# Performance work log

Measured on AMD Instinct MI355X. Metric: run time of the kernel, lower is better.

## Reference

```python
import jax, jax.numpy as jnp
import numpy as np

SCALE = 1.0  # noise std used in the Gaussian log-pdf
HIGH = jax.lax.Precision.HIGHEST


def setup_inputs() -> dict:
    key = jax.random.key(0)
    k1, k2, k3 = jax.random.split(key, 3)
    B, N, D, T = 64, 256, 64, 4096
    data = jax.random.normal(k1, (B, N, D), dtype=jnp.float32)
    targets = jax.random.normal(k2, (B, N), dtype=jnp.float32)
    task_pool = jax.random.normal(k3, (T, D, 1), dtype=jnp.float32)
    return {"data": data, "targets": targets, "task_pool": task_pool}


def reference(data, targets, task_pool):
    # data: [B, N, D], targets: [B, N], task_pool: [T, D, 1]
    W = jnp.squeeze(task_pool).T  # [D, T]
    # Per-point, per-task Gaussian log-likelihood of targets under each task weight.
    Z = jnp.einsum('bnd,dt->bnt', data, W, precision=HIGH)  # [B, N, T]
    resid = targets[:, :, None] - Z
    logp = jax.scipy.stats.norm.logpdf(resid, loc=0.0, scale=SCALE)  # [B, N, T]
    # alpha for step i (i >= 1) is the cumulative log-lik over points 0..i-1.
    cum = jnp.cumsum(logp, axis=1)          # [B, N, T]
    alphas = cum[:, :-1]                    # [B, N-1, T], alphas[:, i-1] = alpha at step i
    post = jax.nn.softmax(alphas, axis=-1)  # posterior over tasks per step
    # MMSE weight per step: posterior-weighted average of task weights.
    w_mmse = jnp.einsum('bit,dt->bid', post, W, precision=HIGH)  # [B, N-1, D]
    preds_rest = jnp.einsum('bid,bid->bi', data[:, 1:], w_mmse)  # [B, N-1]
    # Step 0: prior mean weight (uniform average over task pool).
    pred0 = data[:, 0] @ W.mean(axis=1)  # [B]
    return jnp.concatenate([pred0[:, None], preds_rest], axis=1)  # [B, N]
```

## Files before the change

### kernel.cpp

```cpp
#include <hip/hip_runtime.h>
#include <math.h>

#define BB 64
#define NN 256
#define DD 64
#define TT 4096

#define NCH 16
#define CT (TT/NCH)
#define THREADS 512
#define WAVES 8
#define NB 16
#define NGRP (NN/NB)
#define BN (BB*NN)

typedef __bf16 bf16x8 __attribute__((ext_vector_type(8)));
typedef float  f32x4  __attribute__((ext_vector_type(4)));

#define SHR1 0x111
#define SHR2 0x112
#define SHR4 0x114
#define SHR8 0x118
#define ROR1 0x121
#define ROR2 0x122
#define ROR4 0x124
#define ROR8 0x128

template<int C>
__device__ __forceinline__ float dppf(float x) {
  return __int_as_float(__builtin_amdgcn_update_dpp(
      0, __float_as_int(x), C, 0xf, 0xf, true));
}

__device__ __forceinline__ unsigned short f2bf(float f) {
  unsigned int u = __float_as_uint(f);
  unsigned int r = u + 0x7FFFu + ((u >> 16) & 1u);
  return (unsigned short)(r >> 16);
}
__device__ __forceinline__ float bf2f(unsigned short h) {
  return __uint_as_float(((unsigned int)h) << 16);
}

union FragU { unsigned int u[4]; bf16x8 v; };

__device__ __forceinline__ void merge8(const float4 (*sb)[16], int lane,
                                       float* __restrict__ part, size_t obase) {
  const int col = lane & 15;
  float4 p0 = sb[0][col];
  float M = p0.x, S = p0.y, V = p0.z;
  #pragma unroll
  for (int w = 1; w < WAVES; ++w) {
    float4 pw = sb[w][col];
    float mn = fmaxf(M, pw.x);
    float ea = __expf(M - mn), eb = __expf(pw.x - mn);
    S = fmaf(S, ea, pw.y * eb);
    V = fmaf(V, ea, pw.z * eb);
    M = mn;
  }
  if (lane < 16) {
    const size_t o = (obase + col) * 3;
    part[o] = M; part[o + 1] = S; part[o + 2] = V;
  }
}

__global__ __launch_bounds__(THREADS, 4)
void mmse_phase1(const float* __restrict__ data,
                 const float* __restrict__ targets,
                 const float* __restrict__ Wp,
                 float* __restrict__ part)
{
  const int bx   = blockIdx.x;
  const int b    = bx >> 4;
  const int ch   = bx & 15;
  const int tid  = threadIdx.x;
  const int lane = tid & 63;
  const int wave = tid >> 6;

  __shared__ unsigned int sDH[2][2][64][4];
  __shared__ unsigned int sDL[2][2][64][4];
  __shared__ float4 sbuf[2][WAVES][16];

  bf16x8 aH[2][2], aL[2][2];
  {
    const int tb = ch * CT + wave * 32;
    #pragma unroll
    for (int tile = 0; tile < 2; ++tile) {
      #pragma unroll
      for (int s = 0; s < 2; ++s) {
        const int row = tb + tile * 16 + (lane & 15);
        const int kb  = s * 32 + (lane >> 4) * 8;
        const float* wp = Wp + (size_t)row * DD + kb;
        FragU hu, lu;
        #pragma unroll
        for (int jj = 0; jj < 4; ++jj) {
          const float f0 = wp[2 * jj], f1 = wp[2 * jj + 1];
          const unsigned short h0 = f2bf(f0), h1 = f2bf(f1);
          const unsigned short g0 = f2bf(f0 - bf2f(h0)), g1 = f2bf(f1 - bf2f(h1));
          hu.u[jj] = (unsigned int)h0 | ((unsigned int)h1 << 16);
          lu.u[jj] = (unsigned int)g0 | ((unsigned int)g1 << 16);
        }
        aH[tile][s] = hu.v; aL[tile][s] = lu.v;
      }
    }
  }

  const float* __restrict__ dbase = data + (size_t)b * NN * DD;
  const int sn = tid >> 5, sk2 = tid & 31;
  const int ss = sk2 >> 4, sjp = sk2 & 3;
  const int sl = ((sk2 >> 2) & 3) * 16 + sn;

  {
    const float2 q0 = *(const float2*)(dbase + (size_t)sn * DD + sk2 * 2);
    const unsigned short h0 = f2bf(q0.x), h1 = f2bf(q0.y);
    const unsigned short g0 = f2bf(q0.x - bf2f(h0)), g1 = f2bf(q0.y - bf2f(h1));
    sDH[0][ss][sl][sjp] = (unsigned int)h0 | ((unsigned int)h1 << 16);
    sDL[0][ss][sl][sjp] = (unsigned int)g0 | ((unsigned int)g1 << 16);
  }
  __syncthreads();

  float c8[2][4];
  #pragma unroll
  for (int t8 = 0; t8 < 8; ++t8) c8[t8 >> 2][t8 & 3] = 0.f;

  const size_t obase0 = (size_t)ch * BN + (size_t)b * NN;

  #pragma unroll 1
  for (int g = 0; g < NGRP; ++g) {
    const int buf = g & 1;
    bf16x8 bh0 = *(const bf16x8*)&sDH[buf][0][lane][0];
    bf16x8 bh1 = *(const bf16x8*)&sDH[buf][1][lane][0];
    bf16x8 bl0 = *(const bf16x8*)&sDL[buf][0][lane][0];
    bf16x8 bl1 = *(const bf16x8*)&sDL[buf][1][lane][0];

    float2 q;
    if (g + 1 < NGRP)
      q = *(const float2*)(dbase + (size_t)((g + 1) * NB + sn) * DD + sk2 * 2);

    if (g > 0 && wave == ((g - 1) & 7))
      merge8(sbuf[(g - 1) & 1], lane, part, obase0 + (size_t)(g - 1) * NB);

    f32x4 zz[2];
    zz[0] = (f32x4)(0.f); zz[1] = (f32x4)(0.f);
    zz[0] = __builtin_amdgcn_mfma_f32_16x16x32_bf16(aH[0][0], bh0, zz[0], 0, 0, 0);
    zz[0] = __builtin_amdgcn_mfma_f32_16x16x32_bf16(aH[0][0], bl0, zz[0], 0, 0, 0);
    zz[0] = __builtin_amdgcn_mfma_f32_16x16x32_bf16(aL[0][0], bh0, zz[0], 0, 0, 0);
    zz[0] = __builtin_amdgcn_mfma_f32_16x16x32_bf16(aH[0][1], bh1, zz[0], 0, 0, 0);
    zz[0] = __builtin_amdgcn_mfma_f32_16x16x32_bf16(aH[0][1], bl1, zz[0], 0, 0, 0);
    zz[0] = __builtin_amdgcn_mfma_f32_16x16x32_bf16(aL[0][1], bh1, zz[0], 0, 0, 0);
    zz[1] = __builtin_amdgcn_mfma_f32_16x16x32_bf16(aH[1][0], bh0, zz[1], 0, 0, 0);
    zz[1] = __builtin_amdgcn_mfma_f32_16x16x32_bf16(aH[1][0], bl0, zz[1], 0, 0, 0);
    zz[1] = __builtin_amdgcn_mfma_f32_16x16x32_bf16(aL[1][0], bh0, zz[1], 0, 0, 0);
    zz[1] = __builtin_amdgcn_mfma_f32_16x16x32_bf16(aH[1][1], bh1, zz[1], 0, 0, 0);
    zz[1] = __builtin_amdgcn_mfma_f32_16x16x32_bf16(aH[1][1], bl1, zz[1], 0, 0, 0);
    zz[1] = __builtin_amdgcn_mfma_f32_16x16x32_bf16(aL[1][1], bh1, zz[1], 0, 0, 0);

    const float tg = targets[(size_t)b * NN + g * NB + (lane & 15)];
    float alpha[8];
    float mloc = -3.4e38f;
    #pragma unroll
    for (int t8 = 0; t8 < 8; ++t8) {
      const int tile = t8 >> 2, r = t8 & 3;
      const float z = zz[tile][r];
      const float resid = tg - z;
      const float lp = resid * (resid * -0.5f);
      float x = dppf<SHR1>(lp);
      x += dppf<SHR1>(x);
      x += dppf<SHR2>(x);
      x += dppf<SHR4>(x);
      x += dppf<SHR8>(x);
      float tot = lp;
      tot += dppf<ROR1>(tot);
      tot += dppf<ROR2>(tot);
      tot += dppf<ROR4>(tot);
      tot += dppf<ROR8>(tot);
      const float a_ = c8[tile][r] + x;
      alpha[t8] = a_;
      c8[tile][r] += tot;
      mloc = fmaxf(mloc, a_);
    }
    float m = fmaxf(mloc, __shfl_xor(mloc, 16));
    m = fmaxf(m, __shfl_xor(m, 32));
    float sv = 0.f, vv = 0.f;
    #pragma unroll
    for (int t8 = 0; t8 < 8; ++t8) {
      const float p = __expf(alpha[t8] - m);
      sv += p;
      vv = fmaf(p, zz[t8 >> 2][t8 & 3], vv);
    }
    sv += __shfl_xor(sv, 16); sv += __shfl_xor(sv, 32);
    vv += __shfl_xor(vv, 16); vv += __shfl_xor(vv, 32);
    if (lane < 16) sbuf[buf][wave][lane] = make_float4(m, sv, vv, 0.f);

    if (g + 1 < NGRP) {
      const unsigned short h0 = f2bf(q.x), h1 = f2bf(q.y);
      const unsigned short g0 = f2bf(q.x - bf2f(h0)), g1 = f2bf(q.y - bf2f(h1));
      sDH[buf ^ 1][ss][sl][sjp] = (unsigned int)h0 | ((unsigned int)h1 << 16);
      sDL[buf ^ 1][ss][sl][sjp] = (unsigned int)g0 | ((unsigned int)g1 << 16);
    }
    __syncthreads();
  }

  if (wave == ((NGRP - 1) & 7))
    merge8(sbuf[(NGRP - 1) & 1], lane, part, obase0 + (size_t)(NGRP - 1) * NB);
}

__global__ __launch_bounds__(256)
void mmse_phase2(const float* __restrict__ part, float* __restrict__ out)
{
  const int idx = blockIdx.x * 256 + threadIdx.x;
  float M = -3.4e38f, S = 0.f, V = 0.f;
  #pragma unroll
  for (int ch = 0; ch < NCH; ++ch) {
    const size_t o = ((size_t)ch * BN + idx) * 3;
    const float m2 = part[o], s2 = part[o + 1], v2 = part[o + 2];
    const float mn = fmaxf(M, m2);
    const float ea = __expf(M - mn), eb = __expf(m2 - mn);
    S = fmaf(S, ea, s2 * eb);
    V = fmaf(V, ea, v2 * eb);
    M = mn;
  }
  out[idx] = V / S;
}

extern "C" void kernel_launch(void* const* d_in, const int* in_sizes, int n_in,
                              void* d_out, int out_size, void* d_ws, size_t ws_size,
                              hipStream_t stream)
{
  const float* data      = (const float*)d_in[0];
  const float* targets   = (const float*)d_in[1];
  const float* task_pool = (const float*)d_in[2];
  float* out  = (float*)d_out;
  float* part = (float*)d_ws;

  hipLaunchKernelGGL(mmse_phase1, dim3(BB * NCH), dim3(THREADS), 0, stream,
                     data, targets, task_pool, part);
  hipLaunchKernelGGL(mmse_phase2, dim3(BN / 256), dim3(256), 0, stream,
                     part, out);
}
```

Measured before the change: 130.4 us.

## Pre-split data into swizzled bf16 tiles and stream them with global_load_lds

Adds a pre-pass kernel that converts data once into hi/lo bf16 tiles with an XOR-swizzled layout. Previously each of the 16 task-chunk blocks redid this conversion per batch. The main kernel now copies those tiles straight into LDS with async global_load_lds double-buffering, and stages targets in LDS. It also works in base-2 exponent space, gets the inclusive/total scans from one DPP scan plus a swizzle broadcast, and stores normalized (logsum, mean) pairs in a channel-contiguous layout so phase2 can read them coalesced with two threads per output. The cost is an extra launch plus an extra 2 MB tile write and read through workspace.

```diff
diff --git a/kernel.cpp b/kernel.cpp
--- a/kernel.cpp
+++ b/kernel.cpp
@@ -14,6 +14,11 @@
 #define NGRP (NN/NB)
 #define BN (BB*NN)
 
+#define TILE_BYTES 4096
+#define TILES_BYTES ((size_t)BB*NGRP*TILE_BYTES)
+
+#define NHL2E (-0.72134752044448170368f)
+
 typedef __bf16 bf16x8 __attribute__((ext_vector_type(8)));
 typedef float  f32x4  __attribute__((ext_vector_type(4)));
 
@@ -21,10 +26,6 @@
 #define SHR2 0x112
 #define SHR4 0x114
 #define SHR8 0x118
-#define ROR1 0x121
-#define ROR2 0x122
-#define ROR4 0x124
-#define ROR8 0x128
 
 template<int C>
 __device__ __forceinline__ float dppf(float x) {
@@ -32,6 +33,10 @@
       0, __float_as_int(x), C, 0xf, 0xf, true));
 }
 
+__device__ __forceinline__ float bcast15(float x) {
+  return __int_as_float(__builtin_amdgcn_ds_swizzle(__float_as_int(x), 0x1F0));
+}
+
 __device__ __forceinline__ unsigned short f2bf(float f) {
   unsigned int u = __float_as_uint(f);
   unsigned int r = u + 0x7FFFu + ((u >> 16) & 1u);
@@ -41,30 +46,54 @@
   return __uint_as_float(((unsigned int)h) << 16);
 }
 
+#define GLOAD_LDS16(gp, lp_) \
+  __builtin_amdgcn_global_load_lds((const __attribute__((address_space(1))) void*)(gp), \
+                                   (__attribute__((address_space(3))) void*)(lp_), 16, 0, 0)
+
 union FragU { unsigned int u[4]; bf16x8 v; };
 
-__device__ __forceinline__ void merge8(const float4 (*sb)[16], int lane,
+__global__ __launch_bounds__(256)
+void mmse_phase0(const float* __restrict__ data, unsigned char* __restrict__ tiles)
+{
+  const int e  = blockIdx.x * 256 + threadIdx.x;
+  const int k2 = e & 31;
+  const int n  = (e >> 5) & 255;
+  const int b  = e >> 13;
+  const float2 q = ((const float2*)data)[e];
+  const unsigned short h0 = f2bf(q.x), h1 = f2bf(q.y);
+  const unsigned short g0 = f2bf(q.x - bf2f(h0)), g1 = f2bf(q.y - bf2f(h1));
+  const int nr = n & 15;
+  const int logical = nr * 128 + k2 * 4;
+  const int phys = logical ^ ((nr & 7) << 4);
+  unsigned char* tp = tiles + (size_t)(b * NGRP + (n >> 4)) * TILE_BYTES;
+  *(unsigned int*)(tp + phys)        = (unsigned int)h0 | ((unsigned int)h1 << 16);
+  *(unsigned int*)(tp + 2048 + phys) = (unsigned int)g0 | ((unsigned int)g1 << 16);
+}
+
+__device__ __forceinline__ void merge8(const float2 (*sb)[16], int lane,
                                        float* __restrict__ part, size_t obase) {
   const int col = lane & 15;
-  float4 p0 = sb[0][col];
-  float M = p0.x, S = p0.y, V = p0.z;
+  float2 p0 = sb[0][col];
+  float M = p0.x, S = 1.f, V = p0.y;
   #pragma unroll
   for (int w = 1; w < WAVES; ++w) {
-    float4 pw = sb[w][col];
+    float2 pw = sb[w][col];
     float mn = fmaxf(M, pw.x);
-    float ea = __expf(M - mn), eb = __expf(pw.x - mn);
-    S = fmaf(S, ea, pw.y * eb);
-    V = fmaf(V, ea, pw.z * eb);
+    float ea = __builtin_amdgcn_exp2f(M - mn);
+    float eb = __builtin_amdgcn_exp2f(pw.x - mn);
+    S = S * ea + eb;
+    V = fmaf(V, ea, pw.y * eb);
     M = mn;
   }
   if (lane < 16) {
-    const size_t o = (obase + col) * 3;
-    part[o] = M; part[o + 1] = S; part[o + 2] = V;
+    const size_t o = (obase + (size_t)col * NCH) * 2;
+    part[o]     = M + __log2f(S);
+    part[o + 1] = V / S;
   }
 }
 
 __global__ __launch_bounds__(THREADS, 4)
-void mmse_phase1(const float* __restrict__ data,
+void mmse_phase1(const unsigned char* __restrict__ tiles,
                  const float* __restrict__ targets,
                  const float* __restrict__ Wp,
                  float* __restrict__ part)
@@ -76,9 +105,11 @@
   const int lane = tid & 63;
   const int wave = tid >> 6;
 
-  __shared__ unsigned int sDH[2][2][64][4];
-  __shared__ unsigned int sDL[2][2][64][4];
-  __shared__ float4 sbuf[2][WAVES][16];
+  __shared__ uint4  dbufq[2][256];
+  __shared__ float  tgl[NN];
+  __shared__ float2 sbuf[2][WAVES][16];
+
+  unsigned char* dbufc = (unsigned char*)dbufq;
 
   bf16x8 aH[2][2], aL[2][2];
   {
@@ -104,40 +135,35 @@
     }
   }
 
-  const float* __restrict__ dbase = data + (size_t)b * NN * DD;
-  const int sn = tid >> 5, sk2 = tid & 31;
-  const int ss = sk2 >> 4, sjp = sk2 & 3;
-  const int sl = ((sk2 >> 2) & 3) * 16 + sn;
-
-  {
-    const float2 q0 = *(const float2*)(dbase + (size_t)sn * DD + sk2 * 2);
-    const unsigned short h0 = f2bf(q0.x), h1 = f2bf(q0.y);
-    const unsigned short g0 = f2bf(q0.x - bf2f(h0)), g1 = f2bf(q0.y - bf2f(h1));
-    sDH[0][ss][sl][sjp] = (unsigned int)h0 | ((unsigned int)h1 << 16);
-    sDL[0][ss][sl][sjp] = (unsigned int)g0 | ((unsigned int)g1 << 16);
-  }
+  if (wave == 0)
+    GLOAD_LDS16(targets + (size_t)b * NN + lane * 4, tgl);
+  if (wave < 4)
+    GLOAD_LDS16(tiles + (size_t)(b * NGRP) * TILE_BYTES + wave * 1024 + lane * 16,
+                dbufc + wave * 1024);
   __syncthreads();
 
-  float c8[2][4];
+  float c8[8];
   #pragma unroll
-  for (int t8 = 0; t8 < 8; ++t8) c8[t8 >> 2][t8 & 3] = 0.f;
-
-  const size_t obase0 = (size_t)ch * BN + (size_t)b * NN;
+  for (int i = 0; i < 8; ++i) c8[i] = 0.f;
+
+  const size_t obase0 = (size_t)(b * NN) * NCH + ch;
 
   #pragma unroll 1
   for (int g = 0; g < NGRP; ++g) {
     const int buf = g & 1;
-    bf16x8 bh0 = *(const bf16x8*)&sDH[buf][0][lane][0];
-    bf16x8 bh1 = *(const bf16x8*)&sDH[buf][1][lane][0];
-    bf16x8 bl0 = *(const bf16x8*)&sDL[buf][0][lane][0];
-    bf16x8 bl1 = *(const bf16x8*)&sDL[buf][1][lane][0];
-
-    float2 q;
-    if (g + 1 < NGRP)
-      q = *(const float2*)(dbase + (size_t)((g + 1) * NB + sn) * DD + sk2 * 2);
+    const unsigned char* bp = dbufc + buf * 4096;
+    const int ra = ((lane & 15) * 128 + (lane >> 4) * 16) ^ ((lane & 7) << 4);
+    bf16x8 bh0 = *(const bf16x8*)(bp + ra);
+    bf16x8 bh1 = *(const bf16x8*)(bp + (ra ^ 64));
+    bf16x8 bl0 = *(const bf16x8*)(bp + 2048 + ra);
+    bf16x8 bl1 = *(const bf16x8*)(bp + 2048 + (ra ^ 64));
+
+    if (g + 1 < NGRP && wave < 4)
+      GLOAD_LDS16(tiles + (size_t)(b * NGRP + g + 1) * TILE_BYTES + wave * 1024 + lane * 16,
+                  dbufc + (buf ^ 1) * 4096 + wave * 1024);
 
     if (g > 0 && wave == ((g - 1) & 7))
-      merge8(sbuf[(g - 1) & 1], lane, part, obase0 + (size_t)(g - 1) * NB);
+      merge8(sbuf[(g - 1) & 1], lane, part, obase0 + (size_t)((g - 1) * NB) * NCH);
 
     f32x4 zz[2];
     zz[0] = (f32x4)(0.f); zz[1] = (f32x4)(0.f);
@@ -154,72 +180,83 @@
     zz[1] = __builtin_amdgcn_mfma_f32_16x16x32_bf16(aH[1][1], bl1, zz[1], 0, 0, 0);
     zz[1] = __builtin_amdgcn_mfma_f32_16x16x32_bf16(aL[1][1], bh1, zz[1], 0, 0, 0);
 
-    const float tg = targets[(size_t)b * NN + g * NB + (lane & 15)];
+    const float tgf = tgl[g * 16 + (lane & 15)];
+
     float alpha[8];
     float mloc = -3.4e38f;
     #pragma unroll
-    for (int t8 = 0; t8 < 8; ++t8) {
-      const int tile = t8 >> 2, r = t8 & 3;
-      const float z = zz[tile][r];
-      const float resid = tg - z;
-      const float lp = resid * (resid * -0.5f);
-      float x = dppf<SHR1>(lp);
-      x += dppf<SHR1>(x);
-      x += dppf<SHR2>(x);
-      x += dppf<SHR4>(x);
-      x += dppf<SHR8>(x);
-      float tot = lp;
-      tot += dppf<ROR1>(tot);
-      tot += dppf<ROR2>(tot);
-      tot += dppf<ROR4>(tot);
-      tot += dppf<ROR8>(tot);
-      const float a_ = c8[tile][r] + x;
-      alpha[t8] = a_;
-      c8[tile][r] += tot;
-      mloc = fmaxf(mloc, a_);
+    for (int tile = 0; tile < 2; ++tile) {
+      #pragma unroll
+      for (int r = 0; r < 4; ++r) {
+        const int t8 = tile * 4 + r;
+        const float z  = zz[tile][r];
+        const float rr = tgf - z;
+        const float lp = rr * rr * NHL2E;
+        float x = lp;
+        x += dppf<SHR1>(x);
+        x += dppf<SHR2>(x);
+        x += dppf<SHR4>(x);
+        x += dppf<SHR8>(x);
+        const float tot = bcast15(x);
+        const float a_ = c8[t8] + (x - lp);
+        alpha[t8] = a_;
+        c8[t8] += tot;
+        mloc = fmaxf(mloc, a_);
+      }
     }
     float m = fmaxf(mloc, __shfl_xor(mloc, 16));
     m = fmaxf(m, __shfl_xor(m, 32));
     float sv = 0.f, vv = 0.f;
     #pragma unroll
-    for (int t8 = 0; t8 < 8; ++t8) {
-      const float p = __expf(alpha[t8] - m);
-      sv += p;
-      vv = fmaf(p, zz[t8 >> 2][t8 & 3], vv);
+    for (int tile = 0; tile < 2; ++tile) {
+      #pragma unroll
+      for (int r = 0; r < 4; ++r) {
+        const float p = __builtin_amdgcn_exp2f(alpha[tile * 4 + r] - m);
+        sv += p;
+        vv = fmaf(p, zz[tile][r], vv);
+      }
     }
     sv += __shfl_xor(sv, 16); sv += __shfl_xor(sv, 32);
     vv += __shfl_xor(vv, 16); vv += __shfl_xor(vv, 32);
-    if (lane < 16) sbuf[buf][wave][lane] = make_float4(m, sv, vv, 0.f);
-
-    if (g + 1 < NGRP) {
-      const unsigned short h0 = f2bf(q.x), h1 = f2bf(q.y);
-      const unsigned short g0 = f2bf(q.x - bf2f(h0)), g1 = f2bf(q.y - bf2f(h1));
-      sDH[buf ^ 1][ss][sl][sjp] = (unsigned int)h0 | ((unsigned int)h1 << 16);
-      sDL[buf ^ 1][ss][sl][sjp] = (unsigned int)g0 | ((unsigned int)g1 << 16);
-    }
+    if (lane < 16) {
+      float2 lr;
+      lr.x = m + __log2f(sv);
+      lr.y = vv / sv;
+      sbuf[buf][wave][lane] = lr;
+    }
+
     __syncthreads();
   }
 
   if (wave == ((NGRP - 1) & 7))
-    merge8(sbuf[(NGRP - 1) & 1], lane, part, obase0 + (size_t)(NGRP - 1) * NB);
+    merge8(sbuf[(NGRP - 1) & 1], lane, part, obase0 + (size_t)((NGRP - 1) * NB) * NCH);
 }
 
 __global__ __launch_bounds__(256)
 void mmse_phase2(const float* __restrict__ part, float* __restrict__ out)
 {
-  const int idx = blockIdx.x * 256 + threadIdx.x;
+  const int gid  = blockIdx.x * 256 + threadIdx.x;
+  const int idx  = gid >> 1;
+  const int half = gid & 1;
+  const float2* __restrict__ p = (const float2*)part + (size_t)idx * NCH + half * 8;
   float M = -3.4e38f, S = 0.f, V = 0.f;
   #pragma unroll
-  for (int ch = 0; ch < NCH; ++ch) {
-    const size_t o = ((size_t)ch * BN + idx) * 3;
-    const float m2 = part[o], s2 = part[o + 1], v2 = part[o + 2];
-    const float mn = fmaxf(M, m2);
-    const float ea = __expf(M - mn), eb = __expf(m2 - mn);
-    S = fmaf(S, ea, s2 * eb);
-    V = fmaf(V, ea, v2 * eb);
+  for (int c = 0; c < 8; ++c) {
+    const float2 q = p[c];
+    const float mn = fmaxf(M, q.x);
+    const float ea = __builtin_amdgcn_exp2f(M - mn);
+    const float eb = __builtin_amdgcn_exp2f(q.x - mn);
+    S = fmaf(S, ea, eb);
+    V = fmaf(V, ea, q.y * eb);
     M = mn;
   }
-  out[idx] = V / S;
+  const float m2 = __shfl_xor(M, 1), s2 = __shfl_xor(S, 1), v2 = __shfl_xor(V, 1);
+  const float mn = fmaxf(M, m2);
+  const float ea = __builtin_amdgcn_exp2f(M - mn);
+  const float eb = __builtin_amdgcn_exp2f(m2 - mn);
+  S = fmaf(S, ea, s2 * eb);
+  V = fmaf(V, ea, v2 * eb);
+  if (half == 0) out[idx] = V / S;
 }
 
 extern "C" void kernel_launch(void* const* d_in, const int* in_sizes, int n_in,
@@ -229,11 +266,15 @@
   const float* data      = (const float*)d_in[0];
   const float* targets   = (const float*)d_in[1];
   const float* task_pool = (const float*)d_in[2];
-  float* out  = (float*)d_out;
-  float* part = (float*)d_ws;
-
+  float* out = (float*)d_out;
+
+  unsigned char* tiles = (unsigned char*)d_ws;
+  float* part = (float*)((unsigned char*)d_ws + TILES_BYTES);
+
+  hipLaunchKernelGGL(mmse_phase0, dim3(BB * NN * DD / 2 / 256), dim3(256), 0, stream,
+                     data, tiles);
   hipLaunchKernelGGL(mmse_phase1, dim3(BB * NCH), dim3(THREADS), 0, stream,
-                     data, targets, task_pool, part);
-  hipLaunchKernelGGL(mmse_phase2, dim3(BN / 256), dim3(256), 0, stream,
+                     tiles, targets, task_pool, part);
+  hipLaunchKernelGGL(mmse_phase2, dim3(2 * BN / 256), dim3(256), 0, stream,
                      part, out);
 }
```

Result: faster. 122.2 us (-6.2%).
